# Kernel tuning notes

Measured on AMD Instinct MI355X. Metric: run time of the kernel, lower is better.

The kernel has to match this reference:

```python
import jax, jax.numpy as jnp
import numpy as np
import math

D_MODEL = 1024
N_HEADS = 16
DH = D_MODEL // N_HEADS
THETA = 10000.0


def _rope_tables(S):
    # freqs: (dh/2,)
    inv_freq = 1.0 / (THETA ** (jnp.arange(0, DH, 2, dtype=jnp.float32) / DH))
    ang = jnp.arange(S, dtype=jnp.float32)[:, None] * inv_freq[None, :]  # (S, dh/2)
    cos = jnp.concatenate([jnp.cos(ang), jnp.cos(ang)], axis=-1)  # (S, dh)
    sin = jnp.concatenate([jnp.sin(ang), jnp.sin(ang)], axis=-1)
    return cos, sin


def _apply_rope(x, cos, sin):
    # x: (B, S, H, dh); rotate-half RoPE
    x1, x2 = jnp.split(x, 2, axis=-1)
    rot = jnp.concatenate([-x2, x1], axis=-1)
    c = cos[None, :, None, :]
    s = sin[None, :, None, :]
    return x * c + rot * s


def setup_inputs() -> dict:
    key = jax.random.key(0)
    k1, k2, k3 = jax.random.split(key, 3)
    x = jax.random.normal(k1, (4, 2048, D_MODEL), dtype=jnp.float32)
    qkv = 0.01 * jax.random.normal(k2, (3 * D_MODEL, D_MODEL), dtype=jnp.float32)
    wo = 0.01 * jax.random.normal(k3, (D_MODEL, D_MODEL), dtype=jnp.float32)
    return {"x": x, "qkv": qkv, "wo": wo}


def reference(x, qkv, wo):
    B, S, D = x.shape
    QKV = x @ qkv.T  # (B, S, 3D)
    Q, K, V = jnp.split(QKV, 3, axis=-1)
    q = Q.reshape(B, S, N_HEADS, DH)
    k = K.reshape(B, S, N_HEADS, DH)
    v = V.reshape(B, S, N_HEADS, DH)
    cos, sin = _rope_tables(S)
    q = _apply_rope(q, cos, sin)
    k = _apply_rope(k, cos, sin)
    # (B, H, S, dh)
    q = q.transpose(0, 2, 1, 3)
    k = k.transpose(0, 2, 1, 3)
    v = v.transpose(0, 2, 1, 3)
    scores = jnp.einsum("bhsd,bhtd->bhst", q, k) / math.sqrt(float(DH))
    mask = jnp.tril(jnp.ones((S, S), dtype=scores.dtype))
    scores = scores * mask
    # faithful to original: any exact-zero entry (masked or incidental) -> -inf
    scores = jnp.where(scores == 0.0, -jnp.inf, scores)
    attn = jax.nn.softmax(scores, axis=-1)
    out = jnp.einsum("bhst,bhtd->bhsd", attn, v)  # (B, H, S, dh)
    out = out.transpose(0, 2, 1, 3).reshape(B, S, D)
    return out @ wo.T
```

## Files before the change

### kernel.cpp

```cpp
#include <hip/hip_runtime.h>
#include <math.h>

typedef __bf16 bf16x8 __attribute__((ext_vector_type(8)));
typedef __bf16 bf16x4 __attribute__((ext_vector_type(4)));
typedef float  floatx4 __attribute__((ext_vector_type(4)));
typedef float  floatx2 __attribute__((ext_vector_type(2)));

#define AS1(p) ((__attribute__((address_space(1))) void*)(p))
#define AS3(p) ((__attribute__((address_space(3))) void*)(p))

#define MASKV (-1.0e30f)
#define SOFTMAX_SCALE_LOG2 0.1803368801111244f
#define ROPE_LOG2F 0.4152410118609203f

#define BARRIER do { __builtin_amdgcn_sched_barrier(0); \
                     __builtin_amdgcn_s_barrier(); \
                     __builtin_amdgcn_sched_barrier(0); } while (0)

__global__ __launch_bounds__(256)
void cvt3_kernel(const float* __restrict__ x, const float* __restrict__ qkv,
                 const float* __restrict__ wo, __bf16* __restrict__ xb,
                 __bf16* __restrict__ qkvb, __bf16* __restrict__ wob,
                 float* __restrict__ rt)
{
    const int bi = blockIdx.x;
    if (bi >= 12288) {
        const int e0 = (bi - 12288) * 1024 + threadIdx.x * 4;
#pragma unroll
        for (int j = 0; j < 4; ++j) {
            const int e = e0 + j;
            const int s = e >> 5, d = e & 31;
            const float f = exp2f(-(float)d * ROPE_LOG2F);
            float sn, cs;
            sincosf((float)s * f, &sn, &cs);
            floatx2 t; t[0] = cs; t[1] = sn;
            *(floatx2*)(rt + e * 2) = t;
        }
        return;
    }
    const float* src;
    __bf16* dst;
    int base;
    if (bi < 8192)       { src = x;   dst = xb;   base = bi * 1024; }
    else if (bi < 11264) { src = qkv; dst = qkvb; base = (bi - 8192) * 1024; }
    else                 { src = wo;  dst = wob;  base = (bi - 11264) * 1024; }

    const int i = base + threadIdx.x * 4;
    const floatx4 v = *(const floatx4*)(src + i);
    bf16x4 o;
    o[0] = (__bf16)v[0]; o[1] = (__bf16)v[1];
    o[2] = (__bf16)v[2]; o[3] = (__bf16)v[3];
    *(bf16x4*)(dst + i) = o;
}

__device__ __forceinline__ void gemm_pipe(const __bf16* __restrict__ Ap,
                                          const __bf16* __restrict__ Bp,
                                          const int m0, const int n0,
                                          __bf16* smem, floatx4 (&acc)[4][4])
{
    const int tid  = threadIdx.x;
    const int wave = tid >> 6;
    const int lane = tid & 63;
    const int quad = lane >> 4;
    const int l16  = lane & 15;
    const int wr   = wave >> 2;
    const int wc   = wave & 3;

    const int arow = wr * 32 + l16;
    const int brow = (wc & 1) * 64 + l16;
    const int bsel = (wc >> 1) * 8192;
    const int swz  = (l16 & 7) << 4;
    int coff[2];
    coff[0] = (( (quad << 4))        ^ swz) >> 1;
    coff[1] = ((64 | (quad << 4))    ^ swz) >> 1;

    auto stageA = [&](int buf, int h, int k0) {
        const int o = tid << 4;
        const int r = o >> 7;
        const int c = (o & 127) ^ ((r & 7) << 4);
        const __bf16* src = Ap + (size_t)(m0 + h * 64 + r) * 1024 + k0 + (c >> 1);
        __builtin_amdgcn_global_load_lds(AS1(src),
            AS3(smem + buf * 24576 + h * 4096 + wave * 512), 16, 0, 0);
    };
    auto stageB = [&](int buf, int h, int k0) {
#pragma unroll
        for (int q = 0; q < 2; ++q) {
            const int o = (q * 512 + tid) << 4;
            const int r = o >> 7;
            const int c = (o & 127) ^ ((r & 7) << 4);
            const __bf16* src = Bp + (size_t)(n0 + h * 128 + r) * 1024 + k0 + (c >> 1);
            __builtin_amdgcn_global_load_lds(AS1(src),
                AS3(smem + buf * 24576 + 8192 + h * 8192 + (q * 8 + wave) * 512), 16, 0, 0);
        }
    };

#define RDA(P, qm, fm, ks) (*(const bf16x8*)(smem + (P) * 24576 + (qm) * 4096 \
                             + ((arow + (fm) * 16) << 6) + coff[ks]))
#define RDB(P, g, ks)      (*(const bf16x8*)(smem + (P) * 24576 + 8192 + bsel \
                             + ((brow + (g) * 16) << 6) + coff[ks]))
#define MFMA8(MB, NB, AV, BV) do { \
    _Pragma("unroll") for (int fm_ = 0; fm_ < 2; ++fm_) \
    _Pragma("unroll") for (int gi_ = 0; gi_ < 2; ++gi_) \
    _Pragma("unroll") for (int ks_ = 0; ks_ < 2; ++ks_) \
        acc[(MB) + fm_][(NB) + gi_] = __builtin_amdgcn_mfma_f32_16x16x32_bf16( \
            AV[fm_][ks_], BV[gi_][ks_], acc[(MB) + fm_][(NB) + gi_], 0, 0, 0); \
} while (0)

    stageA(0, 0, 0);  stageB(0, 0, 0);  stageA(0, 1, 0);  stageB(0, 1, 0);
    stageA(1, 0, 64); stageB(1, 0, 64); stageA(1, 1, 64);
    asm volatile("s_waitcnt vmcnt(4)" ::: "memory");
    BARRIER;

    bf16x8 a0[2][2], a1[2][2], b0[2][2], b1[2][2];

#define TILE(JT, P) do { \
    const int kn_ = ((JT) + 2) * 64; \
    _Pragma("unroll") for (int f_ = 0; f_ < 2; ++f_) \
    _Pragma("unroll") for (int k_ = 0; k_ < 2; ++k_) a0[f_][k_] = RDA(P, 0, f_, k_); \
    _Pragma("unroll") for (int g_ = 0; g_ < 2; ++g_) \
    _Pragma("unroll") for (int k_ = 0; k_ < 2; ++k_) b0[g_][k_] = RDB(P, g_, k_); \
    if ((JT) + 1 < 16) stageB(1 - (P), 1, ((JT) + 1) * 64); \
    BARRIER; \
    __builtin_amdgcn_s_setprio(1); MFMA8(0, 0, a0, b0); __builtin_amdgcn_s_setprio(0); \
    BARRIER; \
    _Pragma("unroll") for (int g_ = 0; g_ < 2; ++g_) \
    _Pragma("unroll") for (int k_ = 0; k_ < 2; ++k_) b1[g_][k_] = RDB(P, 2 + g_, k_); \
    if ((JT) + 2 < 16) stageA(P, 0, kn_); \
    BARRIER; \
    __builtin_amdgcn_s_setprio(1); MFMA8(0, 2, a0, b1); __builtin_amdgcn_s_setprio(0); \
    BARRIER; \
    _Pragma("unroll") for (int f_ = 0; f_ < 2; ++f_) \
    _Pragma("unroll") for (int k_ = 0; k_ < 2; ++k_) a1[f_][k_] = RDA(P, 1, f_, k_); \
    if ((JT) + 2 < 16) stageB(P, 0, kn_); \
    BARRIER; \
    __builtin_amdgcn_s_setprio(1); MFMA8(2, 2, a1, b1); __builtin_amdgcn_s_setprio(0); \
    BARRIER; \
    if ((JT) + 2 < 16) stageA(P, 1, kn_); \
    BARRIER; \
    __builtin_amdgcn_s_setprio(1); MFMA8(2, 0, a1, b0); __builtin_amdgcn_s_setprio(0); \
    if ((JT) + 2 < 16)      { asm volatile("s_waitcnt vmcnt(4)" ::: "memory"); } \
    else if ((JT) + 1 < 16) { asm volatile("s_waitcnt vmcnt(0)" ::: "memory"); } \
    BARRIER; \
} while (0)

    for (int it = 0; it < 8; ++it) {
        TILE(2 * it, 0);
        TILE(2 * it + 1, 1);
    }
#undef TILE
#undef RDA
#undef RDB
#undef MFMA8
}

__global__ __launch_bounds__(512, 2)
void gemm_rope_kernel(const __bf16* __restrict__ A, const __bf16* __restrict__ BT,
                      __bf16* __restrict__ Qr, __bf16* __restrict__ Kr,
                      __bf16* __restrict__ Vt, const float* __restrict__ rt)
{
    extern __shared__ __align__(16) __bf16 smem[];
    const int id  = blockIdx.x;
    const int xcd = id & 7, lid = id >> 3;
    const int tm  = xcd * 8 + lid / 12;
    const int tn  = lid % 12;
    const int m0  = tm * 128, n0 = tn * 256;

    floatx4 acc[4][4] = {};
    gemm_pipe(A, BT, m0, n0, smem, acc);

    const int tid  = threadIdx.x;
    const int wave = tid >> 6;
    const int lane = tid & 63;
    const int quad = lane >> 4, l16 = lane & 15;
    const int wr   = wave >> 2, wc = wave & 3;

    const int gn0    = n0 + wc * 64;
    const int region = gn0 >> 10;
    const int h      = (gn0 >> 6) & 15;

    if (region == 2) {
#pragma unroll
        for (int f = 0; f < 4; ++f) {
            const int gm = m0 + (f >> 1) * 64 + wr * 32 + (f & 1) * 16 + quad * 4;
            const int b = gm >> 11, s = gm & 2047;
#pragma unroll
            for (int g = 0; g < 4; ++g) {
                const int d = g * 16 + l16;
                bf16x4 w;
#pragma unroll
                for (int r = 0; r < 4; ++r) w[r] = (__bf16)acc[f][g][r];
                *(bf16x4*)(Vt + ((size_t)(b * 16 + h) * 64 + d) * 2048 + s) = w;
            }
        }
    } else {
        __bf16* dst = region ? Kr : Qr;
        const float sc = region ? 1.0f : SOFTMAX_SCALE_LOG2;
#pragma unroll
        for (int g = 0; g < 2; ++g) {
            const int d1 = g * 16 + l16;
#pragma unroll
            for (int f = 0; f < 4; ++f) {
                const int gm0 = m0 + (f >> 1) * 64 + wr * 32 + (f & 1) * 16 + quad * 4;
                const int b = gm0 >> 11, s0 = gm0 & 2047;
#pragma unroll
                for (int r = 0; r < 4; ++r) {
                    const floatx2 t = *(const floatx2*)(rt + ((s0 + r) * 32 + d1) * 2);
                    const float a1 = acc[f][g][r];
                    const float a2 = acc[f][g + 2][r];
                    __bf16* row = dst + ((size_t)((b * 16 + h) * 2048 + s0 + r)) * 64;
                    row[d1]      = (__bf16)((a1 * t[0] - a2 * t[1]) * sc);
                    row[d1 + 32] = (__bf16)((a2 * t[0] + a1 * t[1]) * sc);
                }
            }
        }
    }
}

__global__ __launch_bounds__(512, 2)
void gemm_bt_kernel(const __bf16* __restrict__ A, const __bf16* __restrict__ BT,
                    float* __restrict__ C)
{
    extern __shared__ __align__(16) __bf16 smem[];
    const int id  = blockIdx.x;
    const int xcd = id & 7, lid = id >> 3;
    const int tm  = xcd * 8 + (lid >> 2);
    const int tn  = lid & 3;
    const int m0  = tm * 128, n0 = tn * 256;

    floatx4 acc[4][4] = {};
    gemm_pipe(A, BT, m0, n0, smem, acc);

    const int tid  = threadIdx.x;
    const int wave = tid >> 6, lane = tid & 63;
    const int quad = lane >> 4, l16 = lane & 15;
    const int wr   = wave >> 2, wc = wave & 3;

#pragma unroll
    for (int f = 0; f < 4; ++f) {
        const int row = m0 + (f >> 1) * 64 + wr * 32 + (f & 1) * 16 + quad * 4;
#pragma unroll
        for (int g = 0; g < 4; ++g) {
            const int col = n0 + wc * 64 + g * 16 + l16;
#pragma unroll
            for (int r = 0; r < 4; ++r)
                C[(size_t)(row + r) * 1024 + col] = acc[f][g][r];
        }
    }
}

__global__ __launch_bounds__(512, 8)
void attn_kernel(const __bf16* __restrict__ Qr, const __bf16* __restrict__ Kr,
                 const __bf16* __restrict__ Vt, __bf16* __restrict__ ctx)
{
    __shared__ __align__(16) __bf16 Ks[64 * 64];
    __shared__ __align__(16) __bf16 Vs[64 * 64];
    __shared__ __align__(16) __bf16 plds[8][16 * 72];

    const int bh   = blockIdx.x;
    const int b    = bh >> 4, h = bh & 15;
    const int tid  = threadIdx.x;
    const int wave = tid >> 6;
    const int lane = tid & 63;
    const int quad = lane >> 4, l16 = lane & 15;
    const int sw   = l16 & 7;

    const __bf16* Qb = Qr + (size_t)bh * 2048 * 64;
    const __bf16* Kb = Kr + (size_t)bh * 2048 * 64;
    const __bf16* Vb = Vt + (size_t)bh * 64 * 2048;
    __bf16* Pw = &plds[wave][0];

    const int row0 = tid >> 3;
    const int jg0  = (tid & 7) ^ (row0 & 7);

    const int tiles[2] = { (int)blockIdx.y, 15 - (int)blockIdx.y };

    for (int pass = 0; pass < 2; ++pass) {
        const int tq    = tiles[pass];
        const int q0b   = tq * 128;
        const int q0    = q0b + wave * 16;
        const int qa    = q0 + l16;
        const int ntile = 2 * tq + 2;

        bf16x8 bq[2];
#pragma unroll
        for (int t = 0; t < 2; ++t)
            bq[t] = *(const bf16x8*)(Qb + (q0 + l16) * 64 + t * 32 + quad * 8);

        floatx4 o[4] = {};
        float lpart = 0.f;

        for (int t = 0; t < ntile; ++t) {
            const int kt = t * 64;
            __builtin_amdgcn_global_load_lds(AS1(Kb + (size_t)(kt + row0) * 64 + jg0 * 8),
                                             AS3(Ks + wave * 512), 16, 0, 0);
            __builtin_amdgcn_global_load_lds(AS1(Vb + (size_t)row0 * 2048 + kt + jg0 * 8),
                                             AS3(Vs + wave * 512), 16, 0, 0);
            asm volatile("s_waitcnt vmcnt(0)" ::: "memory");
            __syncthreads();

            if (kt <= q0 + 15) {
                const bool masked = (t >= ntile - 2);

                floatx4 s[4] = {};
                __builtin_amdgcn_s_setprio(1);
#pragma unroll
                for (int st = 0; st < 4; ++st) {
                    bf16x8 ka0 = *(const bf16x8*)(Ks + (st * 16 + l16) * 64 + ((0 + quad) ^ sw) * 8);
                    bf16x8 ka1 = *(const bf16x8*)(Ks + (st * 16 + l16) * 64 + ((4 + quad) ^ sw) * 8);
                    s[st] = __builtin_amdgcn_mfma_f32_16x16x32_bf16(ka0, bq[0], s[st], 0, 0, 0);
                    s[st] = __builtin_amdgcn_mfma_f32_16x16x32_bf16(ka1, bq[1], s[st], 0, 0, 0);
                }
                __builtin_amdgcn_s_setprio(0);

#pragma unroll
                for (int st = 0; st < 4; ++st) {
                    bf16x4 w;
#pragma unroll
                    for (int r = 0; r < 4; ++r) {
                        float v = s[st][r];
                        if (masked) {
                            const int key = kt + st * 16 + quad * 4 + r;
                            v = (key > qa) ? MASKV : v;
                        }
                        const float p = __builtin_amdgcn_exp2f(v);
                        lpart += p;
                        w[r] = (__bf16)p;
                    }
                    *(bf16x4*)(Pw + l16 * 72 + st * 16 + quad * 4) = w;
                }

                asm volatile("s_waitcnt lgkmcnt(0)" ::: "memory");
                bf16x8 ap0 = *(const bf16x8*)(Pw + l16 * 72 + quad * 8);
                bf16x8 ap1 = *(const bf16x8*)(Pw + l16 * 72 + 32 + quad * 8);

                __builtin_amdgcn_s_setprio(1);
#pragma unroll
                for (int nt = 0; nt < 4; ++nt) {
                    bf16x8 bv0 = *(const bf16x8*)(Vs + (nt * 16 + l16) * 64 + ((0 + quad) ^ sw) * 8);
                    bf16x8 bv1 = *(const bf16x8*)(Vs + (nt * 16 + l16) * 64 + ((4 + quad) ^ sw) * 8);
                    o[nt] = __builtin_amdgcn_mfma_f32_16x16x32_bf16(ap0, bv0, o[nt], 0, 0, 0);
                    o[nt] = __builtin_amdgcn_mfma_f32_16x16x32_bf16(ap1, bv1, o[nt], 0, 0, 0);
                }
                __builtin_amdgcn_s_setprio(0);
            }

            __syncthreads();
        }

        float l = lpart;
        l += __shfl_xor(l, 16, 64);
        l += __shfl_xor(l, 32, 64);
        float lr[4];
#pragma unroll
        for (int r = 0; r < 4; ++r)
            lr[r] = __shfl(l, quad * 4 + r, 64);
#pragma unroll
        for (int nt = 0; nt < 4; ++nt)
#pragma unroll
            for (int r = 0; r < 4; ++r) {
                const int srow = q0 + quad * 4 + r;
                const float inv_l = 1.0f / fmaxf(lr[r], 1e-20f);
                ctx[((size_t)(b * 2048 + srow)) * 1024 + h * 64 + nt * 16 + l16] =
                    (__bf16)(o[nt][r] * inv_l);
            }
    }
}

extern "C" void kernel_launch(void* const* d_in, const int* in_sizes, int n_in,
                              void* d_out, int out_size, void* d_ws, size_t ws_size,
                              hipStream_t stream)
{
    const float* x   = (const float*)d_in[0];
    const float* qkv = (const float*)d_in[1];
    const float* wo  = (const float*)d_in[2];
    float* out = (float*)d_out;

    char* ws = (char*)d_ws;
    const size_t MB = 1024 * 1024;
    __bf16* xb   = (__bf16*)(ws);
    __bf16* qkvb = (__bf16*)(ws + 16 * MB);
    __bf16* wob  = (__bf16*)(ws + 22 * MB);
    __bf16* Qr   = (__bf16*)(ws + 24 * MB);
    __bf16* Kr   = (__bf16*)(ws + 40 * MB);
    __bf16* Vt   = (__bf16*)(ws + 56 * MB);
    __bf16* ctx  = (__bf16*)(ws + 72 * MB);
    float*  rt   = (float*) (ws + 88 * MB);

    hipFuncSetAttribute((const void*)gemm_rope_kernel,
                        hipFuncAttributeMaxDynamicSharedMemorySize, 98304);
    hipFuncSetAttribute((const void*)gemm_bt_kernel,
                        hipFuncAttributeMaxDynamicSharedMemorySize, 98304);

    cvt3_kernel<<<12352, 256, 0, stream>>>(x, qkv, wo, xb, qkvb, wob, rt);
    gemm_rope_kernel<<<768, 512, 98304, stream>>>(xb, qkvb, Qr, Kr, Vt, rt);
    attn_kernel<<<dim3(64, 8), 512, 0, stream>>>(Qr, Kr, Vt, ctx);
    gemm_bt_kernel<<<256, 512, 98304, stream>>>(ctx, wob, out);
}
```

Baseline: 253.6 us.

## Shrink attention blocks to 64 queries and register-prefetch next K/V tile

The attention kernel now uses 256-thread blocks covering 64-query tiles on a 64x16 grid, still pairing tiles t and 31-t for causal load balance. Per-wave wasted iterations on fully masked tiles go away, and only the final tile is masked. Direct global-to-LDS loads are replaced by register staging that fetches the next K/V tile while the current one is computed, hiding global latency. The cost is extra registers and LDS store instructions, and more blocks each reloading K/V.

```diff
diff --git a/kernel.cpp b/kernel.cpp
--- a/kernel.cpp
+++ b/kernel.cpp
@@ -248,13 +248,13 @@
     }
 }
 
-__global__ __launch_bounds__(512, 8)
+__global__ __launch_bounds__(256, 4)
 void attn_kernel(const __bf16* __restrict__ Qr, const __bf16* __restrict__ Kr,
                  const __bf16* __restrict__ Vt, __bf16* __restrict__ ctx)
 {
     __shared__ __align__(16) __bf16 Ks[64 * 64];
     __shared__ __align__(16) __bf16 Vs[64 * 64];
-    __shared__ __align__(16) __bf16 plds[8][16 * 72];
+    __shared__ __align__(16) __bf16 plds[4][16 * 72];
 
     const int bh   = blockIdx.x;
     const int b    = bh >> 4, h = bh & 15;
@@ -269,17 +269,22 @@
     const __bf16* Vb = Vt + (size_t)bh * 64 * 2048;
     __bf16* Pw = &plds[wave][0];
 
-    const int row0 = tid >> 3;
-    const int jg0  = (tid & 7) ^ (row0 & 7);
-
-    const int tiles[2] = { (int)blockIdx.y, 15 - (int)blockIdx.y };
+    const int row0 = tid >> 3, jg0 = (tid & 7) ^ (row0 & 7);
+    const int c1   = 256 + tid;
+    const int row1 = c1 >> 3, jg1 = (c1 & 7) ^ (row1 & 7);
+
+    const __bf16* pK0 = Kb + (size_t)row0 * 64 + jg0 * 8;
+    const __bf16* pK1 = Kb + (size_t)row1 * 64 + jg1 * 8;
+    const __bf16* pV0 = Vb + (size_t)row0 * 2048 + jg0 * 8;
+    const __bf16* pV1 = Vb + (size_t)row1 * 2048 + jg1 * 8;
+
+    const int tiles[2] = { (int)blockIdx.y, 31 - (int)blockIdx.y };
 
     for (int pass = 0; pass < 2; ++pass) {
         const int tq    = tiles[pass];
-        const int q0b   = tq * 128;
-        const int q0    = q0b + wave * 16;
+        const int q0    = tq * 64 + wave * 16;
         const int qa    = q0 + l16;
-        const int ntile = 2 * tq + 2;
+        const int ntile = tq + 1;
 
         bf16x8 bq[2];
 #pragma unroll
@@ -289,62 +294,75 @@
         floatx4 o[4] = {};
         float lpart = 0.f;
 
+        bf16x8 rk0 = *(const bf16x8*)pK0;
+        bf16x8 rk1 = *(const bf16x8*)pK1;
+        bf16x8 rv0 = *(const bf16x8*)pV0;
+        bf16x8 rv1 = *(const bf16x8*)pV1;
+
+        __syncthreads();
+
         for (int t = 0; t < ntile; ++t) {
-            const int kt = t * 64;
-            __builtin_amdgcn_global_load_lds(AS1(Kb + (size_t)(kt + row0) * 64 + jg0 * 8),
-                                             AS3(Ks + wave * 512), 16, 0, 0);
-            __builtin_amdgcn_global_load_lds(AS1(Vb + (size_t)row0 * 2048 + kt + jg0 * 8),
-                                             AS3(Vs + wave * 512), 16, 0, 0);
             asm volatile("s_waitcnt vmcnt(0)" ::: "memory");
-            __syncthreads();
-
-            if (kt <= q0 + 15) {
-                const bool masked = (t >= ntile - 2);
-
-                floatx4 s[4] = {};
-                __builtin_amdgcn_s_setprio(1);
-#pragma unroll
-                for (int st = 0; st < 4; ++st) {
-                    bf16x8 ka0 = *(const bf16x8*)(Ks + (st * 16 + l16) * 64 + ((0 + quad) ^ sw) * 8);
-                    bf16x8 ka1 = *(const bf16x8*)(Ks + (st * 16 + l16) * 64 + ((4 + quad) ^ sw) * 8);
-                    s[st] = __builtin_amdgcn_mfma_f32_16x16x32_bf16(ka0, bq[0], s[st], 0, 0, 0);
-                    s[st] = __builtin_amdgcn_mfma_f32_16x16x32_bf16(ka1, bq[1], s[st], 0, 0, 0);
+            *(bf16x8*)(Ks + tid * 8)        = rk0;
+            *(bf16x8*)(Ks + 2048 + tid * 8) = rk1;
+            *(bf16x8*)(Vs + tid * 8)        = rv0;
+            *(bf16x8*)(Vs + 2048 + tid * 8) = rv1;
+            asm volatile("s_waitcnt lgkmcnt(0)" ::: "memory");
+            BARRIER;
+
+            if (t + 1 < ntile) {
+                rk0 = *(const bf16x8*)(pK0 + (size_t)(t + 1) * 4096);
+                rk1 = *(const bf16x8*)(pK1 + (size_t)(t + 1) * 4096);
+                rv0 = *(const bf16x8*)(pV0 + (t + 1) * 64);
+                rv1 = *(const bf16x8*)(pV1 + (t + 1) * 64);
+            }
+
+            const int  kt     = t * 64;
+            const bool masked = (t == ntile - 1);
+
+            floatx4 s[4] = {};
+            __builtin_amdgcn_s_setprio(1);
+#pragma unroll
+            for (int st = 0; st < 4; ++st) {
+                bf16x8 ka0 = *(const bf16x8*)(Ks + (st * 16 + l16) * 64 + ((0 + quad) ^ sw) * 8);
+                bf16x8 ka1 = *(const bf16x8*)(Ks + (st * 16 + l16) * 64 + ((4 + quad) ^ sw) * 8);
+                s[st] = __builtin_amdgcn_mfma_f32_16x16x32_bf16(ka0, bq[0], s[st], 0, 0, 0);
+                s[st] = __builtin_amdgcn_mfma_f32_16x16x32_bf16(ka1, bq[1], s[st], 0, 0, 0);
+            }
+            __builtin_amdgcn_s_setprio(0);
+
+#pragma unroll
+            for (int st = 0; st < 4; ++st) {
+                bf16x4 w;
+#pragma unroll
+                for (int r = 0; r < 4; ++r) {
+                    float v = s[st][r];
+                    if (masked) {
+                        const int key = kt + st * 16 + quad * 4 + r;
+                        v = (key > qa) ? MASKV : v;
+                    }
+                    const float p = __builtin_amdgcn_exp2f(v);
+                    lpart += p;
+                    w[r] = (__bf16)p;
                 }
-                __builtin_amdgcn_s_setprio(0);
-
-#pragma unroll
-                for (int st = 0; st < 4; ++st) {
-                    bf16x4 w;
-#pragma unroll
-                    for (int r = 0; r < 4; ++r) {
-                        float v = s[st][r];
-                        if (masked) {
-                            const int key = kt + st * 16 + quad * 4 + r;
-                            v = (key > qa) ? MASKV : v;
-                        }
-                        const float p = __builtin_amdgcn_exp2f(v);
-                        lpart += p;
-                        w[r] = (__bf16)p;
-                    }
-                    *(bf16x4*)(Pw + l16 * 72 + st * 16 + quad * 4) = w;
-                }
-
-                asm volatile("s_waitcnt lgkmcnt(0)" ::: "memory");
-                bf16x8 ap0 = *(const bf16x8*)(Pw + l16 * 72 + quad * 8);
-                bf16x8 ap1 = *(const bf16x8*)(Pw + l16 * 72 + 32 + quad * 8);
-
-                __builtin_amdgcn_s_setprio(1);
-#pragma unroll
-                for (int nt = 0; nt < 4; ++nt) {
-                    bf16x8 bv0 = *(const bf16x8*)(Vs + (nt * 16 + l16) * 64 + ((0 + quad) ^ sw) * 8);
-                    bf16x8 bv1 = *(const bf16x8*)(Vs + (nt * 16 + l16) * 64 + ((4 + quad) ^ sw) * 8);
-                    o[nt] = __builtin_amdgcn_mfma_f32_16x16x32_bf16(ap0, bv0, o[nt], 0, 0, 0);
-                    o[nt] = __builtin_amdgcn_mfma_f32_16x16x32_bf16(ap1, bv1, o[nt], 0, 0, 0);
-                }
-                __builtin_amdgcn_s_setprio(0);
-            }
-
-            __syncthreads();
+                *(bf16x4*)(Pw + l16 * 72 + st * 16 + quad * 4) = w;
+            }
+
+            asm volatile("s_waitcnt lgkmcnt(0)" ::: "memory");
+            bf16x8 ap0 = *(const bf16x8*)(Pw + l16 * 72 + quad * 8);
+            bf16x8 ap1 = *(const bf16x8*)(Pw + l16 * 72 + 32 + quad * 8);
+
+            __builtin_amdgcn_s_setprio(1);
+#pragma unroll
+            for (int nt = 0; nt < 4; ++nt) {
+                bf16x8 bv0 = *(const bf16x8*)(Vs + (nt * 16 + l16) * 64 + ((0 + quad) ^ sw) * 8);
+                bf16x8 bv1 = *(const bf16x8*)(Vs + (nt * 16 + l16) * 64 + ((4 + quad) ^ sw) * 8);
+                o[nt] = __builtin_amdgcn_mfma_f32_16x16x32_bf16(ap0, bv0, o[nt], 0, 0, 0);
+                o[nt] = __builtin_amdgcn_mfma_f32_16x16x32_bf16(ap1, bv1, o[nt], 0, 0, 0);
+            }
+            __builtin_amdgcn_s_setprio(0);
+
+            BARRIER;
         }
 
         float l = lpart;
@@ -393,6 +411,6 @@
 
     cvt3_kernel<<<12352, 256, 0, stream>>>(x, qkv, wo, xb, qkvb, wob, rt);
     gemm_rope_kernel<<<768, 512, 98304, stream>>>(xb, qkvb, Qr, Kr, Vt, rt);
-    attn_kernel<<<dim3(64, 8), 512, 0, stream>>>(Qr, Kr, Vt, ctx);
+    attn_kernel<<<dim3(64, 16), 256, 0, stream>>>(Qr, Kr, Vt, ctx);
     gemm_bt_kernel<<<256, 512, 98304, stream>>>(ctx, wob, out);
 }
```

Result: faster. 237.7 us (-6.3%).
